# Kernel optimization log

Measured on AMD Instinct MI355X. Metric: run time of the kernel, lower is better.

## Reference

```python
import jax, jax.numpy as jnp
import numpy as np

NUM_HEADS = 8
CHUNK = 2
TAU = 2.0

# --- LIF neuron with ATan surrogate gradient (spikingjelly MultiStepLIFNode, hard reset to 0, detach_reset) ---
@jax.custom_vjp
def spike(x):
    return (x >= 0.0).astype(x.dtype)

def _spike_fwd(x):
    return spike(x), x

def _spike_bwd(x, g):
    alpha = 2.0
    sg = (alpha / 2.0) / (1.0 + (jnp.pi / 2.0 * alpha * x) ** 2)
    return (g * sg,)

spike.defvjp(_spike_fwd, _spike_bwd)

def lif(x_seq, v_th=1.0):
    # x_seq: [T, ...]; v' = v + (x - v)/tau ; spike if v' >= v_th ; hard reset v=0 (reset path detached)
    def step(v, x):
        v = v + (x - v) / TAU
        s = spike(v - v_th)
        v = v * (1.0 - jax.lax.stop_gradient(s))
        return v, s
    _, s = jax.lax.scan(step, jnp.zeros_like(x_seq[0]), x_seq)
    return s

def conv1x1_bn(x, W, scale, bias, conv_bias=None):
    # 1x1 conv over channel dim + eval-mode BN (per-channel affine)
    y = jnp.einsum('tbchw,dc->tbdhw', x, W)
    if conv_bias is not None:
        y = y + conv_bias[None, None, :, None, None]
    return y * scale[None, None, :, None, None] + bias[None, None, :, None, None]


def setup_inputs() -> dict:
    key = jax.random.key(0)
    ks = jax.random.split(key, 16)
    T, B, C, H, W = 4, 32, 512, 16, 16
    s = 1.0 / np.sqrt(C)
    return {
        'x': jax.random.normal(ks[0], (T, B, C, H, W), jnp.float32),
        'Wq': jax.random.normal(ks[1], (C, C), jnp.float32) * s,
        'q_scale': jax.random.uniform(ks[2], (C,), jnp.float32, 0.5, 1.5),
        'q_bias': jax.random.normal(ks[3], (C,), jnp.float32) * 0.1,
        'Wk': jax.random.normal(ks[4], (C, C), jnp.float32) * s,
        'k_scale': jax.random.uniform(ks[5], (C,), jnp.float32, 0.5, 1.5),
        'k_bias': jax.random.normal(ks[6], (C,), jnp.float32) * 0.1,
        'Wv': jax.random.normal(ks[7], (C, C), jnp.float32) * s,
        'v_scale': jax.random.uniform(ks[8], (C,), jnp.float32, 0.5, 1.5),
        'v_bias': jax.random.normal(ks[9], (C,), jnp.float32) * 0.1,
        'Wp': jax.random.normal(ks[10], (C, C), jnp.float32) * s,
        'bp': jax.random.normal(ks[11], (C,), jnp.float32) * 0.1,
        'p_scale': jax.random.uniform(ks[12], (C,), jnp.float32, 0.5, 1.5),
        'p_bias': jax.random.normal(ks[13], (C,), jnp.float32) * 0.1,
    }


def reference(x, Wq, q_scale, q_bias, Wk, k_scale, k_bias, Wv, v_scale, v_bias, Wp, bp, p_scale, p_bias):
    T, B, C, H, W = x.shape
    N = H * W
    hd = C // NUM_HEADS
    identity = x

    xs = lif(x)  # shortcut_lif

    def qkv_branch(W_, sc, bi):
        y = lif(conv1x1_bn(xs, W_, sc, bi))           # [T,B,C,H,W] spikes
        # flatten(3).transpose(-1,-2).reshape(...heads...).permute == split C, swap N/hd
        return jnp.swapaxes(y.reshape(T, B, NUM_HEADS, hd, N), -1, -2)  # [T,B,h,N,hd]

    q = qkv_branch(Wq, q_scale, q_bias)
    k = qkv_branch(Wk, k_scale, k_bias)
    v = qkv_branch(Wv, v_scale, v_bias)

    # STAtten: temporal chunking, linear attention q @ (k^T v)
    scaling = 1.0 / H
    nc = T // CHUNK

    def to_chunks(y):  # [T,B,h,N,hd] -> [nc,B,h,CHUNK*N,hd]
        return (y.reshape(nc, CHUNK, B, NUM_HEADS, N, hd)
                 .transpose(0, 2, 3, 1, 4, 5)
                 .reshape(nc, B, NUM_HEADS, CHUNK * N, hd))

    qc, kc, vc = to_chunks(q), to_chunks(k), to_chunks(v)
    attn = jnp.einsum('nbhsd,nbhse->nbhde', kc, vc) * scaling   # [nc,B,h,hd,hd]
    out = jnp.einsum('nbhsd,nbhde->nbhse', qc, attn)            # [nc,B,h,CHUNK*N,hd]
    out = (out.reshape(nc, B, NUM_HEADS, CHUNK, N, hd)
              .transpose(0, 3, 1, 2, 4, 5)
              .reshape(T, B, NUM_HEADS, N, hd))

    x2 = jnp.swapaxes(out, -1, -2).reshape(T, B, C, N)          # [T,B,C,N]
    x2 = lif(x2, v_th=0.5).reshape(T, B, C, H, W)               # attn_lif

    x3 = conv1x1_bn(x2, Wp, p_scale, p_bias, conv_bias=bp)      # proj conv+BN
    return x3 + identity, v
```

## Files before the change

kernel.cpp:

```cpp
#include <hip/hip_runtime.h>

typedef unsigned short ushort_t;
typedef unsigned char u8;
typedef short bf16x8 __attribute__((ext_vector_type(8)));
typedef float f32x4 __attribute__((ext_vector_type(4)));

#define T_DIM 4
#define B_DIM 32
#define C_DIM 512
#define N_DIM 256

__device__ __forceinline__ float bf2f(ushort_t u) {
  union { unsigned int i; float f; } x;
  x.i = ((unsigned int)u) << 16;
  return x.f;
}
__device__ __forceinline__ ushort_t f2bf(float f) {
  unsigned int u = __float_as_uint(f);
  u = (u + 0x7FFFu + ((u >> 16) & 1u)) >> 16;
  return (ushort_t)u;
}

__global__ __launch_bounds__(256) void k0_split(
    const float* __restrict__ Wq, const float* __restrict__ Wk,
    const float* __restrict__ Wv, const float* __restrict__ Wp,
    ushort_t* __restrict__ Sqkv, ushort_t* __restrict__ Sp)
{
  int gid = blockIdx.x * 256 + threadIdx.x;
  int w = gid >> 15;
  int off = (gid & 32767) * 8;
  const float* src = (w == 0) ? Wq : ((w == 1) ? Wk : ((w == 2) ? Wv : Wp));
  ushort_t* dst = (w < 3) ? (Sqkv + (size_t)w * 3 * 262144) : Sp;
  float wv[8];
  *(float4*)&wv[0] = *(const float4*)(src + off);
  *(float4*)&wv[4] = *(const float4*)(src + off + 4);
  ushort_t hi[8], mi[8], lo[8];
#pragma unroll
  for (int i = 0; i < 8; i++) {
    float f = wv[i];
    ushort_t h = f2bf(f);  float r  = f - bf2f(h);
    ushort_t m = f2bf(r);  float r2 = r - bf2f(m);
    ushort_t l = f2bf(r2);
    hi[i] = h; mi[i] = m; lo[i] = l;
  }
  *(uint4*)(dst + off)              = *(uint4*)&hi[0];
  *(uint4*)(dst + 262144 + off)     = *(uint4*)&mi[0];
  *(uint4*)(dst + 2 * 262144 + off) = *(uint4*)&lo[0];
}

__global__ __launch_bounds__(256) void k1_shortcut_lif(
    const float* __restrict__ x, u8* __restrict__ xsT8)
{
  const int n0 = blockIdx.x * 64;
  const int c0 = blockIdx.y * 64;
  const int b  = blockIdx.z;
  __shared__ u8 sm[64][80];
  const int tid = threadIdx.x;
  const int r  = tid >> 2;
  const int j0 = (tid & 3) * 16;
  float v[16];
#pragma unroll
  for (int i = 0; i < 16; i++) v[i] = 0.f;
  for (int t = 0; t < T_DIM; t++) {
    const float* xp = x + ((((size_t)t * B_DIM + b) * C_DIM) + c0 + r) * N_DIM + n0 + j0;
    float xv[16];
    *(float4*)&xv[0]  = *(const float4*)xp;
    *(float4*)&xv[4]  = *(const float4*)(xp + 4);
    *(float4*)&xv[8]  = *(const float4*)(xp + 8);
    *(float4*)&xv[12] = *(const float4*)(xp + 12);
    __syncthreads();
#pragma unroll
    for (int i = 0; i < 16; i++) {
      float nv = v[i] + (xv[i] - v[i]) * 0.5f;
      bool s = (nv >= 1.0f);
      v[i] = s ? 0.f : nv;
      sm[j0 + i][r] = s ? (u8)1 : (u8)0;
    }
    __syncthreads();
    union { uint4 u; u8 b[16]; } ov;
#pragma unroll
    for (int i = 0; i < 16; i++) ov.b[i] = sm[r][j0 + i];
    u8* op = xsT8 + ((((size_t)t * B_DIM + b) * N_DIM) + n0 + r) * C_DIM + c0 + j0;
    *(uint4*)op = ov.u;
  }
}

__global__ __launch_bounds__(512, 4) void k2_qkv(
    const u8* __restrict__ xsT8, const ushort_t* __restrict__ Sqkv,
    const float* __restrict__ qsc, const float* __restrict__ qbi,
    const float* __restrict__ ksc, const float* __restrict__ kbi,
    const float* __restrict__ vsc, const float* __restrict__ vbi,
    u8* __restrict__ qs8, u8* __restrict__ ks8, float* __restrict__ vout)
{
  const int nt = blockIdx.x;
  const int mt = blockIdx.y;
  const int b  = blockIdx.z;
  const int branch = mt >> 3;
  const int mloc = (mt & 7) * 64;
  const ushort_t* Ws = Sqkv + (size_t)branch * 3 * 262144;
  const float* scp = (branch == 0) ? qsc : ((branch == 1) ? ksc : vsc);
  const float* bip = (branch == 0) ? qbi : ((branch == 1) ? kbi : vbi);

  __shared__ ushort_t As3[2][3][64][32];
  __shared__ ushort_t Bs[2][128][32];

  const int tid  = threadIdx.x;
  const int lane = tid & 63;
  const int wave = tid >> 6;
  const int wrow = (wave >> 1) * 16;
  const int wcol = (wave & 1) * 64;
  const int frow = lane & 15;
  const int fsl  = lane >> 4;

  const u8* Bb0 = xsT8 + ((size_t)b * N_DIM + nt * 128) * C_DIM;

  const int ach0 = tid;
  const int ap0 = ach0 >> 8, ar0 = (ach0 & 255) >> 2, asl0 = ach0 & 3;
  const int ach1 = tid + 512;
  const int ap1 = ach1 >> 8, ar1 = (ach1 & 255) >> 2, asl1 = ach1 & 3;
  const int brow = tid >> 1, bsl0 = (tid & 1) * 2;
  uint4 pa0, pa1, pb;

#define K2_LOAD(s_) { int t_ = (s_) >> 4; int kb_ = ((s_) & 15) * 32;                     \
    pa0 = *(const uint4*)(Ws + (size_t)ap0 * 262144 + (size_t)(mloc + ar0) * 512 + kb_ + asl0 * 8); \
    if (tid < 256) {                                                                       \
      pa1 = *(const uint4*)(Ws + (size_t)ap1 * 262144 + (size_t)(mloc + ar1) * 512 + kb_ + asl1 * 8); \
      pb  = *(const uint4*)(Bb0 + (size_t)t_ * B_DIM * N_DIM * C_DIM + (size_t)brow * 512 + kb_ + bsl0 * 8); \
    } }

#define K2_WRITE(buf_) {                                                                   \
    *(uint4*)&As3[buf_][ap0][ar0][(asl0 ^ ((ar0 >> 1) & 3)) * 8] = pa0;                    \
    if (tid < 256) {                                                                       \
      *(uint4*)&As3[buf_][ap1][ar1][(asl1 ^ ((ar1 >> 1) & 3)) * 8] = pa1;                  \
      union { uint4 u; u8 bb[16]; } rw_; rw_.u = pb;                                       \
      ushort_t tmp_[16];                                                                   \
      _Pragma("unroll") for (int z_ = 0; z_ < 16; z_++) tmp_[z_] = rw_.bb[z_] ? (ushort_t)0x3F80u : (ushort_t)0u; \
      int sw_ = (brow >> 1) & 3;                                                           \
      *(uint4*)&Bs[buf_][brow][((bsl0) ^ sw_) * 8]     = *(uint4*)&tmp_[0];                \
      *(uint4*)&Bs[buf_][brow][((bsl0 + 1) ^ sw_) * 8] = *(uint4*)&tmp_[8];                \
    } }

  f32x4 acc[4];
  float vst[16];
#pragma unroll
  for (int i = 0; i < 16; i++) vst[i] = 0.f;
#pragma unroll
  for (int i = 0; i < 4; i++) acc[i] = (f32x4){0.f, 0.f, 0.f, 0.f};

  const int crow0 = (lane >> 4) * 4;
  const int cn    = lane & 15;
  float sc4[4], bi4[4];
#pragma unroll
  for (int r = 0; r < 4; r++) {
    int c = mloc + wrow + crow0 + r;
    sc4[r] = scp[c]; bi4[r] = bip[c];
  }

  K2_LOAD(0); K2_WRITE(0); __syncthreads();

  for (int s = 0; s < 64; s++) {
    const int cur = s & 1;
    if (s < 63) K2_LOAD(s + 1);
    bf16x8 bfr[4];
#pragma unroll
    for (int j = 0; j < 4; j++) {
      int row = wcol + j * 16 + frow;
      bfr[j] = *(const bf16x8*)&Bs[cur][row][(fsl ^ ((row >> 1) & 3)) * 8];
    }
    int arow = wrow + frow;
    int asw  = (fsl ^ ((arow >> 1) & 3)) * 8;
#pragma unroll
    for (int p = 0; p < 3; p++) {
      bf16x8 af = *(const bf16x8*)&As3[cur][p][arow][asw];
#pragma unroll
      for (int j = 0; j < 4; j++)
        acc[j] = __builtin_amdgcn_mfma_f32_16x16x32_bf16(af, bfr[j], acc[j], 0, 0, 0);
    }
    if (s < 63) K2_WRITE((s + 1) & 1);
    __syncthreads();

    if ((s & 15) == 15) {
      const int t = s >> 4;
      const size_t tb = (size_t)t * B_DIM + b;
      if (branch < 2) {
        u8* dst = (branch == 0) ? qs8 : ks8;
#pragma unroll
        for (int r = 0; r < 4; r++) {
          int c = mloc + wrow + crow0 + r;
#pragma unroll
          for (int j = 0; j < 4; j++) {
            int n = nt * 128 + wcol + j * 16 + cn;
            float y = acc[j][r] * sc4[r] + bi4[r];
            int vi = j * 4 + r;
            float v = vst[vi];
            v = v + (y - v) * 0.5f;
            bool sp = (v >= 1.0f);
            vst[vi] = sp ? 0.f : v;
            dst[(tb * C_DIM + c) * N_DIM + n] = sp ? (u8)1 : (u8)0;
          }
        }
      } else {
        const int hv = mloc >> 6;
        const int d0 = wrow + crow0;
#pragma unroll
        for (int j = 0; j < 4; j++) {
          int n = nt * 128 + wcol + j * 16 + cn;
          float4 o;
          float ov[4];
#pragma unroll
          for (int r = 0; r < 4; r++) {
            float y = acc[j][r] * sc4[r] + bi4[r];
            int vi = j * 4 + r;
            float v = vst[vi];
            v = v + (y - v) * 0.5f;
            bool sp = (v >= 1.0f);
            vst[vi] = sp ? 0.f : v;
            ov[r] = sp ? 1.0f : 0.0f;
          }
          o.x = ov[0]; o.y = ov[1]; o.z = ov[2]; o.w = ov[3];
          *(float4*)(vout + ((tb * 8 + hv) * N_DIM + n) * 64 + d0) = o;
        }
      }
#pragma unroll
      for (int i = 0; i < 4; i++) acc[i] = (f32x4){0.f, 0.f, 0.f, 0.f};
    }
  }
#undef K2_LOAD
#undef K2_WRITE
}

__global__ __launch_bounds__(256) void k3_attn(
    const u8* __restrict__ ks8, const float* __restrict__ vsp,
    float* __restrict__ attn)
{
  const int h  = blockIdx.x;
  const int b  = blockIdx.y;
  const int ch = blockIdx.z;
  __shared__ u8 KtT[64][80];
  __shared__ u8 Vt[64][80];
  const int tid = threadIdx.x;
  const int d0 = (tid >> 4) * 4;
  const int e0 = (tid & 15) * 4;
  float a[16];
#pragma unroll
  for (int i = 0; i < 16; i++) a[i] = 0.f;

  for (int tt = 0; tt < 2; tt++) {
    int t = ch * 2 + tt;
    for (int n0 = 0; n0 < 256; n0 += 64) {
      __syncthreads();
      {
        int d  = tid >> 2;
        int s0 = (tid & 3) * 16;
        union { uint4 u; u8 bvec[16]; } kb;
        kb.u = *(const uint4*)(ks8 + ((((size_t)t * B_DIM + b) * C_DIM) + h * 64 + d) * N_DIM + n0 + s0);
#pragma unroll
        for (int i = 0; i < 16; i++) KtT[s0 + i][d] = kb.bvec[i];
      }
      {
        const float* vb = vsp + ((((size_t)t * B_DIM + b) * 8 + h) * N_DIM + n0) * 64;
#pragma unroll
        for (int u = 0; u < 4; u++) {
          int chunk = tid + u * 256;
          int row = chunk >> 4;
          int eo  = (chunk & 15) * 4;
          float4 v4 = *(const float4*)(vb + (size_t)row * 64 + eo);
          Vt[row][eo + 0] = (u8)(v4.x != 0.f);
          Vt[row][eo + 1] = (u8)(v4.y != 0.f);
          Vt[row][eo + 2] = (u8)(v4.z != 0.f);
          Vt[row][eo + 3] = (u8)(v4.w != 0.f);
        }
      }
      __syncthreads();
      for (int s = 0; s < 64; s++) {
        uchar4 kb = *(const uchar4*)&KtT[s][d0];
        float kv[4] = { (float)kb.x, (float)kb.y, (float)kb.z, (float)kb.w };
        uchar4 vr = *(const uchar4*)&Vt[s][e0];
        float vv[4] = { (float)vr.x, (float)vr.y, (float)vr.z, (float)vr.w };
#pragma unroll
        for (int i = 0; i < 4; i++)
#pragma unroll
          for (int j = 0; j < 4; j++) a[i * 4 + j] += kv[i] * vv[j];
      }
    }
  }
  float* ap = attn + ((((size_t)ch * B_DIM + b) * 8 + h) * 64 + d0) * 64 + e0;
#pragma unroll
  for (int i = 0; i < 4; i++)
#pragma unroll
    for (int j = 0; j < 4; j++)
      ap[i * 64 + j] = a[i * 4 + j] * 0.0625f;
}

__global__ __launch_bounds__(256) void k4_out_lif(
    const u8* __restrict__ qs8, const float* __restrict__ attn,
    u8* __restrict__ x2sT8)
{
  const int h  = blockIdx.x;
  const int b  = blockIdx.y;
  const int nc = blockIdx.z;
  __shared__ float At[64][68];
  __shared__ u8 Qt[64][80];
  const int tid = threadIdx.x;
  const int e0 = (tid >> 4) * 4;
  const int n0 = (tid & 15) * 4;
  float vst[16];
#pragma unroll
  for (int i = 0; i < 16; i++) vst[i] = 0.f;

  for (int t = 0; t < T_DIM; t++) {
    if ((t & 1) == 0) {
      __syncthreads();
      const float* ap = attn + ((((size_t)(t >> 1) * B_DIM + b) * 8) + h) * 4096;
      int dr = tid >> 2;
      int co = (tid & 3) * 16;
#pragma unroll
      for (int u = 0; u < 4; u++)
        *(float4*)&At[dr][co + u * 4] = *(const float4*)(ap + dr * 64 + co + u * 4);
    }
    __syncthreads();
    {
      int d  = tid >> 2;
      int so = (tid & 3) * 16;
      *(uint4*)&Qt[d][so] =
        *(const uint4*)(qs8 + ((((size_t)t * B_DIM + b) * C_DIM) + h * 64 + d) * N_DIM + nc * 64 + so);
    }
    __syncthreads();
    float acc[16];
#pragma unroll
    for (int i = 0; i < 16; i++) acc[i] = 0.f;
    for (int d = 0; d < 64; d++) {
      float4 av = *(const float4*)&At[d][e0];
      float avv[4] = { av.x, av.y, av.z, av.w };
      uchar4 qr = *(const uchar4*)&Qt[d][n0];
      float qv[4] = { (float)qr.x, (float)qr.y, (float)qr.z, (float)qr.w };
#pragma unroll
      for (int i = 0; i < 4; i++)
#pragma unroll
        for (int j = 0; j < 4; j++) acc[i * 4 + j] += avv[i] * qv[j];
    }
#pragma unroll
    for (int j = 0; j < 4; j++) {
      u8 sv[4];
#pragma unroll
      for (int i = 0; i < 4; i++) {
        int vi = i * 4 + j;
        float y = acc[i * 4 + j];
        float nv = vst[vi] + (y - vst[vi]) * 0.5f;
        bool s = (nv >= 0.5f);
        vst[vi] = s ? 0.f : nv;
        sv[i] = s ? (u8)1 : (u8)0;
      }
      int n = nc * 64 + n0 + j;
      u8* op = x2sT8 + ((((size_t)t * B_DIM + b) * N_DIM) + n) * C_DIM + h * 64 + e0;
      *(uchar4*)op = make_uchar4(sv[0], sv[1], sv[2], sv[3]);
    }
  }
}

__global__ __launch_bounds__(512, 4) void k5_proj(
    const u8* __restrict__ x2sT8, const ushort_t* __restrict__ Sp,
    const float* __restrict__ bp, const float* __restrict__ psc,
    const float* __restrict__ pbi,
    const float* __restrict__ x, float* __restrict__ out0)
{
  const int nt = blockIdx.x;
  const int mt = blockIdx.y;
  const int tb = blockIdx.z;
  const int mloc = mt * 64;

  __shared__ ushort_t As3[2][3][64][32];
  __shared__ ushort_t Bs[2][128][32];

  const int tid  = threadIdx.x;
  const int lane = tid & 63;
  const int wave = tid >> 6;
  const int wrow = (wave >> 1) * 16;
  const int wcol = (wave & 1) * 64;
  const int frow = lane & 15;
  const int fsl  = lane >> 4;

  const u8* Bb = x2sT8 + ((size_t)tb * N_DIM + nt * 128) * C_DIM;

  const int ach0 = tid;
  const int ap0 = ach0 >> 8, ar0 = (ach0 & 255) >> 2, asl0 = ach0 & 3;
  const int ach1 = tid + 512;
  const int ap1 = ach1 >> 8, ar1 = (ach1 & 255) >> 2, asl1 = ach1 & 3;
  const int brow = tid >> 1, bsl0 = (tid & 1) * 2;
  uint4 pa0, pa1, pb;

#define K5_LOAD(s_) { int kb_ = (s_) * 32;                                                 \
    pa0 = *(const uint4*)(Sp + (size_t)ap0 * 262144 + (size_t)(mloc + ar0) * 512 + kb_ + asl0 * 8); \
    if (tid < 256) {                                                                       \
      pa1 = *(const uint4*)(Sp + (size_t)ap1 * 262144 + (size_t)(mloc + ar1) * 512 + kb_ + asl1 * 8); \
      pb  = *(const uint4*)(Bb + (size_t)brow * 512 + kb_ + bsl0 * 8);                     \
    } }

#define K5_WRITE(buf_) {                                                                   \
    *(uint4*)&As3[buf_][ap0][ar0][(asl0 ^ ((ar0 >> 1) & 3)) * 8] = pa0;                    \
    if (tid < 256) {                                                                       \
      *(uint4*)&As3[buf_][ap1][ar1][(asl1 ^ ((ar1 >> 1) & 3)) * 8] = pa1;                  \
      union { uint4 u; u8 bb[16]; } rw_; rw_.u = pb;                                       \
      ushort_t tmp_[16];                                                                   \
      _Pragma("unroll") for (int z_ = 0; z_ < 16; z_++) tmp_[z_] = rw_.bb[z_] ? (ushort_t)0x3F80u : (ushort_t)0u; \
      int sw_ = (brow >> 1) & 3;                                                           \
      *(uint4*)&Bs[buf_][brow][((bsl0) ^ sw_) * 8]     = *(uint4*)&tmp_[0];                \
      *(uint4*)&Bs[buf_][brow][((bsl0 + 1) ^ sw_) * 8] = *(uint4*)&tmp_[8];                \
    } }

  f32x4 acc[4];
#pragma unroll
  for (int i = 0; i < 4; i++) acc[i] = (f32x4){0.f, 0.f, 0.f, 0.f};

  K5_LOAD(0); K5_WRITE(0); __syncthreads();

  for (int s = 0; s < 16; s++) {
    const int cur = s & 1;
    if (s < 15) K5_LOAD(s + 1);
    bf16x8 bfr[4];
#pragma unroll
    for (int j = 0; j < 4; j++) {
      int row = wcol + j * 16 + frow;
      bfr[j] = *(const bf16x8*)&Bs[cur][row][(fsl ^ ((row >> 1) & 3)) * 8];
    }
    int arow = wrow + frow;
    int asw  = (fsl ^ ((arow >> 1) & 3)) * 8;
#pragma unroll
    for (int p = 0; p < 3; p++) {
      bf16x8 af = *(const bf16x8*)&As3[cur][p][arow][asw];
#pragma unroll
      for (int j = 0; j < 4; j++)
        acc[j] = __builtin_amdgcn_mfma_f32_16x16x32_bf16(af, bfr[j], acc[j], 0, 0, 0);
    }
    if (s < 15) K5_WRITE((s + 1) & 1);
    __syncthreads();
  }

  const int crow0 = (lane >> 4) * 4;
  const int cn    = lane & 15;
#pragma unroll
  for (int r = 0; r < 4; r++) {
    int c = mloc + wrow + crow0 + r;
    float scf = psc[c];
    float bif = pbi[c];
    float bpf = bp[c];
#pragma unroll
    for (int j = 0; j < 4; j++) {
      int n = nt * 128 + wcol + j * 16 + cn;
      size_t idx = ((size_t)tb * C_DIM + c) * N_DIM + n;
      out0[idx] = (acc[j][r] + bpf) * scf + bif + x[idx];
    }
  }
#undef K5_LOAD
#undef K5_WRITE
}

extern "C" void kernel_launch(void* const* d_in, const int* in_sizes, int n_in,
                              void* d_out, int out_size, void* d_ws, size_t ws_size,
                              hipStream_t stream) {
  const float* x   = (const float*)d_in[0];
  const float* Wq  = (const float*)d_in[1];
  const float* qsc = (const float*)d_in[2];
  const float* qbi = (const float*)d_in[3];
  const float* Wk  = (const float*)d_in[4];
  const float* ksc = (const float*)d_in[5];
  const float* kbi = (const float*)d_in[6];
  const float* Wv  = (const float*)d_in[7];
  const float* vsc = (const float*)d_in[8];
  const float* vbi = (const float*)d_in[9];
  const float* Wp  = (const float*)d_in[10];
  const float* bp  = (const float*)d_in[11];
  const float* psc = (const float*)d_in[12];
  const float* pbi = (const float*)d_in[13];

  float* out0 = (float*)d_out;
  float* out1 = out0 + 16777216;

  const size_t M16 = 16u * 1024u * 1024u;
  char* o0 = (char*)d_out;
  char* ws = (char*)d_ws;

  u8*       xsT8  = (u8*)(o0);
  u8*       qs8   = (u8*)(o0 + M16);
  u8*       ks8   = (u8*)(o0 + 2 * M16);
  ushort_t* Sqkv  = (ushort_t*)(o0 + 3 * M16);
  float*    attn  = (float*)(o0);
  u8*       x2sT8 = (u8*)(ws);
  ushort_t* Sp    = (ushort_t*)(ws + M16);

  hipLaunchKernelGGL(k0_split,        dim3(512),        dim3(256), 0, stream,
                     Wq, Wk, Wv, Wp, Sqkv, Sp);
  hipLaunchKernelGGL(k1_shortcut_lif, dim3(4, 8, 32),   dim3(256), 0, stream, x, xsT8);
  hipLaunchKernelGGL(k2_qkv,          dim3(2, 24, 32),  dim3(512), 0, stream,
                     xsT8, Sqkv, qsc, qbi, ksc, kbi, vsc, vbi, qs8, ks8, out1);
  hipLaunchKernelGGL(k3_attn,         dim3(8, 32, 2),   dim3(256), 0, stream, ks8, out1, attn);
  hipLaunchKernelGGL(k4_out_lif,      dim3(8, 32, 4),   dim3(256), 0, stream, qs8, attn, x2sT8);
  hipLaunchKernelGGL(k5_proj,         dim3(2, 8, 128),  dim3(512), 0, stream,
                     x2sT8, Sp, bp, psc, pbi, x, out0);
}
```

Before: 521.0 us.

## Use direct global-to-LDS loads and wider N tiles in QKV and proj GEMMs

Both the QKV and projection GEMM kernels now stage A and B tiles with global_load_lds (direct global-to-LDS, bypassing registers) instead of register loads followed by LDS writes. The B operand stays as u8 spikes in LDS and is expanded to bf16 at fragment-read time with perm and multiply. The N tile is doubled to 256 so each block covers the full spatial dim, which halves the grid and doubles the accumulators per wave. The XOR swizzle on LDS is dropped, which can add bank conflicts. Register pressure also rises, and the grid is smaller (768 and 1024 blocks).

```diff
diff --git a/kernel.cpp b/kernel.cpp
--- a/kernel.cpp
+++ b/kernel.cpp
@@ -19,6 +19,12 @@
   unsigned int u = __float_as_uint(f);
   u = (u + 0x7FFFu + ((u >> 16) & 1u)) >> 16;
   return (ushort_t)u;
+}
+
+__device__ __forceinline__ void gload16(const void* g, void* l) {
+  __builtin_amdgcn_global_load_lds(
+      (const __attribute__((address_space(1))) unsigned int*)g,
+      (__attribute__((address_space(3))) unsigned int*)l, 16, 0, 0);
 }
 
 __global__ __launch_bounds__(256) void k0_split(
@@ -92,60 +98,51 @@
     const float* __restrict__ vsc, const float* __restrict__ vbi,
     u8* __restrict__ qs8, u8* __restrict__ ks8, float* __restrict__ vout)
 {
-  const int nt = blockIdx.x;
-  const int mt = blockIdx.y;
-  const int b  = blockIdx.z;
+  const int mt = blockIdx.x;
+  const int b  = blockIdx.y;
   const int branch = mt >> 3;
   const int mloc = (mt & 7) * 64;
   const ushort_t* Ws = Sqkv + (size_t)branch * 3 * 262144;
   const float* scp = (branch == 0) ? qsc : ((branch == 1) ? ksc : vsc);
   const float* bip = (branch == 0) ? qbi : ((branch == 1) ? kbi : vbi);
 
-  __shared__ ushort_t As3[2][3][64][32];
-  __shared__ ushort_t Bs[2][128][32];
+  __shared__ alignas(16) ushort_t As[2][3][64][32];
+  __shared__ alignas(16) u8 Bs8[2][256][32];
 
   const int tid  = threadIdx.x;
   const int lane = tid & 63;
   const int wave = tid >> 6;
   const int wrow = (wave >> 1) * 16;
-  const int wcol = (wave & 1) * 64;
+  const int wcol = (wave & 1) * 128;
   const int frow = lane & 15;
   const int fsl  = lane >> 4;
 
-  const u8* Bb0 = xsT8 + ((size_t)b * N_DIM + nt * 128) * C_DIM;
-
-  const int ach0 = tid;
-  const int ap0 = ach0 >> 8, ar0 = (ach0 & 255) >> 2, asl0 = ach0 & 3;
-  const int ach1 = tid + 512;
-  const int ap1 = ach1 >> 8, ar1 = (ach1 & 255) >> 2, asl1 = ach1 & 3;
-  const int brow = tid >> 1, bsl0 = (tid & 1) * 2;
-  uint4 pa0, pa1, pb;
-
-#define K2_LOAD(s_) { int t_ = (s_) >> 4; int kb_ = ((s_) & 15) * 32;                     \
-    pa0 = *(const uint4*)(Ws + (size_t)ap0 * 262144 + (size_t)(mloc + ar0) * 512 + kb_ + asl0 * 8); \
-    if (tid < 256) {                                                                       \
-      pa1 = *(const uint4*)(Ws + (size_t)ap1 * 262144 + (size_t)(mloc + ar1) * 512 + kb_ + asl1 * 8); \
-      pb  = *(const uint4*)(Bb0 + (size_t)t_ * B_DIM * N_DIM * C_DIM + (size_t)brow * 512 + kb_ + bsl0 * 8); \
-    } }
-
-#define K2_WRITE(buf_) {                                                                   \
-    *(uint4*)&As3[buf_][ap0][ar0][(asl0 ^ ((ar0 >> 1) & 3)) * 8] = pa0;                    \
-    if (tid < 256) {                                                                       \
-      *(uint4*)&As3[buf_][ap1][ar1][(asl1 ^ ((ar1 >> 1) & 3)) * 8] = pa1;                  \
-      union { uint4 u; u8 bb[16]; } rw_; rw_.u = pb;                                       \
-      ushort_t tmp_[16];                                                                   \
-      _Pragma("unroll") for (int z_ = 0; z_ < 16; z_++) tmp_[z_] = rw_.bb[z_] ? (ushort_t)0x3F80u : (ushort_t)0u; \
-      int sw_ = (brow >> 1) & 3;                                                           \
-      *(uint4*)&Bs[buf_][brow][((bsl0) ^ sw_) * 8]     = *(uint4*)&tmp_[0];                \
-      *(uint4*)&Bs[buf_][brow][((bsl0 + 1) ^ sw_) * 8] = *(uint4*)&tmp_[8];                \
-    } }
-
-  f32x4 acc[4];
-  float vst[16];
-#pragma unroll
-  for (int i = 0; i < 16; i++) vst[i] = 0.f;
-#pragma unroll
-  for (int i = 0; i < 4; i++) acc[i] = (f32x4){0.f, 0.f, 0.f, 0.f};
+  const u8* Bb0 = xsT8 + (size_t)b * N_DIM * C_DIM;
+
+  const int a0p = wave >> 2, a0q = wave & 3;
+  const int arl = lane >> 2;
+  const int acl = (lane & 3) * 8;
+  const int brl = lane >> 1;
+  const int bcl = (lane & 1) * 16;
+  const int cbx = (wave < 4) ? (4 + wave) : (wave - 4);
+
+#define K2_STAGE(s_) {                                                                     \
+    const int t_ = (s_) >> 4; const int kb_ = ((s_) & 15) * 32; const int bf_ = (s_) & 1;  \
+    gload16(Ws + (size_t)a0p * 262144 + (size_t)(mloc + a0q * 16 + arl) * 512 + kb_ + acl, \
+            &As[bf_][a0p][a0q * 16][0]);                                                   \
+    if (wave < 4)                                                                          \
+      gload16(Ws + 2 * 262144 + (size_t)(mloc + wave * 16 + arl) * 512 + kb_ + acl,        \
+              &As[bf_][2][wave * 16][0]);                                                  \
+    gload16(Bb0 + (size_t)t_ * (B_DIM * N_DIM * C_DIM) + (size_t)(cbx * 32 + brl) * 512 + kb_ + bcl, \
+            &Bs8[bf_][cbx * 32][0]);                                                       \
+  }
+
+  f32x4 acc[8];
+  float vst[32];
+#pragma unroll
+  for (int i = 0; i < 32; i++) vst[i] = 0.f;
+#pragma unroll
+  for (int j = 0; j < 8; j++) acc[j] = (f32x4){0.f, 0.f, 0.f, 0.f};
 
   const int crow0 = (lane >> 4) * 4;
   const int cn    = lane & 15;
@@ -156,28 +153,31 @@
     sc4[r] = scp[c]; bi4[r] = bip[c];
   }
 
-  K2_LOAD(0); K2_WRITE(0); __syncthreads();
+  K2_STAGE(0);
+  __syncthreads();
 
   for (int s = 0; s < 64; s++) {
     const int cur = s & 1;
-    if (s < 63) K2_LOAD(s + 1);
-    bf16x8 bfr[4];
-#pragma unroll
-    for (int j = 0; j < 4; j++) {
-      int row = wcol + j * 16 + frow;
-      bfr[j] = *(const bf16x8*)&Bs[cur][row][(fsl ^ ((row >> 1) & 3)) * 8];
-    }
-    int arow = wrow + frow;
-    int asw  = (fsl ^ ((arow >> 1) & 3)) * 8;
-#pragma unroll
-    for (int p = 0; p < 3; p++) {
-      bf16x8 af = *(const bf16x8*)&As3[cur][p][arow][asw];
-#pragma unroll
-      for (int j = 0; j < 4; j++)
-        acc[j] = __builtin_amdgcn_mfma_f32_16x16x32_bf16(af, bfr[j], acc[j], 0, 0, 0);
-    }
-    if (s < 63) K2_WRITE((s + 1) & 1);
-    __syncthreads();
+    if (s < 63) K2_STAGE(s + 1);
+
+    bf16x8 af[3];
+    const int ar = wrow + frow;
+#pragma unroll
+    for (int p = 0; p < 3; p++) af[p] = *(const bf16x8*)&As[cur][p][ar][fsl * 8];
+
+#pragma unroll
+    for (int j = 0; j < 8; j++) {
+      const int row = wcol + j * 16 + frow;
+      uint2 raw = *(const uint2*)&Bs8[cur][row][fsl * 8];
+      union { bf16x8 v; unsigned int u[4]; } bu;
+      bu.u[0] = __builtin_amdgcn_perm(0u, raw.x, 0x05010400u) * 0x3F80u;
+      bu.u[1] = __builtin_amdgcn_perm(0u, raw.x, 0x07030602u) * 0x3F80u;
+      bu.u[2] = __builtin_amdgcn_perm(0u, raw.y, 0x05010400u) * 0x3F80u;
+      bu.u[3] = __builtin_amdgcn_perm(0u, raw.y, 0x07030602u) * 0x3F80u;
+#pragma unroll
+      for (int p = 0; p < 3; p++)
+        acc[j] = __builtin_amdgcn_mfma_f32_16x16x32_bf16(af[p], bu.v, acc[j], 0, 0, 0);
+    }
 
     if ((s & 15) == 15) {
       const int t = s >> 4;
@@ -186,12 +186,12 @@
         u8* dst = (branch == 0) ? qs8 : ks8;
 #pragma unroll
         for (int r = 0; r < 4; r++) {
-          int c = mloc + wrow + crow0 + r;
-#pragma unroll
-          for (int j = 0; j < 4; j++) {
-            int n = nt * 128 + wcol + j * 16 + cn;
+          const int c = mloc + wrow + crow0 + r;
+#pragma unroll
+          for (int j = 0; j < 8; j++) {
+            const int n = wcol + j * 16 + cn;
             float y = acc[j][r] * sc4[r] + bi4[r];
-            int vi = j * 4 + r;
+            const int vi = j * 4 + r;
             float v = vst[vi];
             v = v + (y - v) * 0.5f;
             bool sp = (v >= 1.0f);
@@ -203,30 +203,29 @@
         const int hv = mloc >> 6;
         const int d0 = wrow + crow0;
 #pragma unroll
-        for (int j = 0; j < 4; j++) {
-          int n = nt * 128 + wcol + j * 16 + cn;
-          float4 o;
+        for (int j = 0; j < 8; j++) {
+          const int n = wcol + j * 16 + cn;
           float ov[4];
 #pragma unroll
           for (int r = 0; r < 4; r++) {
             float y = acc[j][r] * sc4[r] + bi4[r];
-            int vi = j * 4 + r;
+            const int vi = j * 4 + r;
             float v = vst[vi];
             v = v + (y - v) * 0.5f;
             bool sp = (v >= 1.0f);
             vst[vi] = sp ? 0.f : v;
             ov[r] = sp ? 1.0f : 0.0f;
           }
-          o.x = ov[0]; o.y = ov[1]; o.z = ov[2]; o.w = ov[3];
-          *(float4*)(vout + ((tb * 8 + hv) * N_DIM + n) * 64 + d0) = o;
+          *(float4*)(vout + ((tb * 8 + hv) * N_DIM + n) * 64 + d0) =
+              make_float4(ov[0], ov[1], ov[2], ov[3]);
         }
       }
 #pragma unroll
-      for (int i = 0; i < 4; i++) acc[i] = (f32x4){0.f, 0.f, 0.f, 0.f};
-    }
-  }
-#undef K2_LOAD
-#undef K2_WRITE
+      for (int j = 0; j < 8; j++) acc[j] = (f32x4){0.f, 0.f, 0.f, 0.f};
+    }
+    __syncthreads();
+  }
+#undef K2_STAGE
 }
 
 __global__ __launch_bounds__(256) void k3_attn(
@@ -364,75 +363,69 @@
     const float* __restrict__ pbi,
     const float* __restrict__ x, float* __restrict__ out0)
 {
-  const int nt = blockIdx.x;
-  const int mt = blockIdx.y;
-  const int tb = blockIdx.z;
+  const int mt = blockIdx.x;
+  const int tb = blockIdx.y;
   const int mloc = mt * 64;
 
-  __shared__ ushort_t As3[2][3][64][32];
-  __shared__ ushort_t Bs[2][128][32];
+  __shared__ alignas(16) ushort_t As[2][3][64][32];
+  __shared__ alignas(16) u8 Bs8[2][256][32];
 
   const int tid  = threadIdx.x;
   const int lane = tid & 63;
   const int wave = tid >> 6;
   const int wrow = (wave >> 1) * 16;
-  const int wcol = (wave & 1) * 64;
+  const int wcol = (wave & 1) * 128;
   const int frow = lane & 15;
   const int fsl  = lane >> 4;
 
-  const u8* Bb = x2sT8 + ((size_t)tb * N_DIM + nt * 128) * C_DIM;
-
-  const int ach0 = tid;
-  const int ap0 = ach0 >> 8, ar0 = (ach0 & 255) >> 2, asl0 = ach0 & 3;
-  const int ach1 = tid + 512;
-  const int ap1 = ach1 >> 8, ar1 = (ach1 & 255) >> 2, asl1 = ach1 & 3;
-  const int brow = tid >> 1, bsl0 = (tid & 1) * 2;
-  uint4 pa0, pa1, pb;
-
-#define K5_LOAD(s_) { int kb_ = (s_) * 32;                                                 \
-    pa0 = *(const uint4*)(Sp + (size_t)ap0 * 262144 + (size_t)(mloc + ar0) * 512 + kb_ + asl0 * 8); \
-    if (tid < 256) {                                                                       \
-      pa1 = *(const uint4*)(Sp + (size_t)ap1 * 262144 + (size_t)(mloc + ar1) * 512 + kb_ + asl1 * 8); \
-      pb  = *(const uint4*)(Bb + (size_t)brow * 512 + kb_ + bsl0 * 8);                     \
-    } }
-
-#define K5_WRITE(buf_) {                                                                   \
-    *(uint4*)&As3[buf_][ap0][ar0][(asl0 ^ ((ar0 >> 1) & 3)) * 8] = pa0;                    \
-    if (tid < 256) {                                                                       \
-      *(uint4*)&As3[buf_][ap1][ar1][(asl1 ^ ((ar1 >> 1) & 3)) * 8] = pa1;                  \
-      union { uint4 u; u8 bb[16]; } rw_; rw_.u = pb;                                       \
-      ushort_t tmp_[16];                                                                   \
-      _Pragma("unroll") for (int z_ = 0; z_ < 16; z_++) tmp_[z_] = rw_.bb[z_] ? (ushort_t)0x3F80u : (ushort_t)0u; \
-      int sw_ = (brow >> 1) & 3;                                                           \
-      *(uint4*)&Bs[buf_][brow][((bsl0) ^ sw_) * 8]     = *(uint4*)&tmp_[0];                \
-      *(uint4*)&Bs[buf_][brow][((bsl0 + 1) ^ sw_) * 8] = *(uint4*)&tmp_[8];                \
-    } }
-
-  f32x4 acc[4];
-#pragma unroll
-  for (int i = 0; i < 4; i++) acc[i] = (f32x4){0.f, 0.f, 0.f, 0.f};
-
-  K5_LOAD(0); K5_WRITE(0); __syncthreads();
+  const u8* Bb = x2sT8 + (size_t)tb * N_DIM * C_DIM;
+
+  const int a0p = wave >> 2, a0q = wave & 3;
+  const int arl = lane >> 2;
+  const int acl = (lane & 3) * 8;
+  const int brl = lane >> 1;
+  const int bcl = (lane & 1) * 16;
+  const int cbx = (wave < 4) ? (4 + wave) : (wave - 4);
+
+#define K5_STAGE(s_) {                                                                     \
+    const int kb_ = (s_) * 32; const int bf_ = (s_) & 1;                                   \
+    gload16(Sp + (size_t)a0p * 262144 + (size_t)(mloc + a0q * 16 + arl) * 512 + kb_ + acl, \
+            &As[bf_][a0p][a0q * 16][0]);                                                   \
+    if (wave < 4)                                                                          \
+      gload16(Sp + 2 * 262144 + (size_t)(mloc + wave * 16 + arl) * 512 + kb_ + acl,        \
+              &As[bf_][2][wave * 16][0]);                                                  \
+    gload16(Bb + (size_t)(cbx * 32 + brl) * 512 + kb_ + bcl, &Bs8[bf_][cbx * 32][0]);      \
+  }
+
+  f32x4 acc[8];
+#pragma unroll
+  for (int j = 0; j < 8; j++) acc[j] = (f32x4){0.f, 0.f, 0.f, 0.f};
+
+  K5_STAGE(0);
+  __syncthreads();
 
   for (int s = 0; s < 16; s++) {
     const int cur = s & 1;
-    if (s < 15) K5_LOAD(s + 1);
-    bf16x8 bfr[4];
-#pragma unroll
-    for (int j = 0; j < 4; j++) {
-      int row = wcol + j * 16 + frow;
-      bfr[j] = *(const bf16x8*)&Bs[cur][row][(fsl ^ ((row >> 1) & 3)) * 8];
-    }
-    int arow = wrow + frow;
-    int asw  = (fsl ^ ((arow >> 1) & 3)) * 8;
-#pragma unroll
-    for (int p = 0; p < 3; p++) {
-      bf16x8 af = *(const bf16x8*)&As3[cur][p][arow][asw];
-#pragma unroll
-      for (int j = 0; j < 4; j++)
-        acc[j] = __builtin_amdgcn_mfma_f32_16x16x32_bf16(af, bfr[j], acc[j], 0, 0, 0);
-    }
-    if (s < 15) K5_WRITE((s + 1) & 1);
+    if (s < 15) K5_STAGE(s + 1);
+
+    bf16x8 af[3];
+    const int ar = wrow + frow;
+#pragma unroll
+    for (int p = 0; p < 3; p++) af[p] = *(const bf16x8*)&As[cur][p][ar][fsl * 8];
+
+#pragma unroll
+    for (int j = 0; j < 8; j++) {
+      const int row = wcol + j * 16 + frow;
+      uint2 raw = *(const uint2*)&Bs8[cur][row][fsl * 8];
+      union { bf16x8 v; unsigned int u[4]; } bu;
+      bu.u[0] = __builtin_amdgcn_perm(0u, raw.x, 0x05010400u) * 0x3F80u;
+      bu.u[1] = __builtin_amdgcn_perm(0u, raw.x, 0x07030602u) * 0x3F80u;
+      bu.u[2] = __builtin_amdgcn_perm(0u, raw.y, 0x05010400u) * 0x3F80u;
+      bu.u[3] = __builtin_amdgcn_perm(0u, raw.y, 0x07030602u) * 0x3F80u;
+#pragma unroll
+      for (int p = 0; p < 3; p++)
+        acc[j] = __builtin_amdgcn_mfma_f32_16x16x32_bf16(af[p], bu.v, acc[j], 0, 0, 0);
+    }
     __syncthreads();
   }
 
@@ -440,19 +433,18 @@
   const int cn    = lane & 15;
 #pragma unroll
   for (int r = 0; r < 4; r++) {
-    int c = mloc + wrow + crow0 + r;
-    float scf = psc[c];
-    float bif = pbi[c];
-    float bpf = bp[c];
-#pragma unroll
-    for (int j = 0; j < 4; j++) {
-      int n = nt * 128 + wcol + j * 16 + cn;
-      size_t idx = ((size_t)tb * C_DIM + c) * N_DIM + n;
+    const int c = mloc + wrow + crow0 + r;
+    const float scf = psc[c];
+    const float bif = pbi[c];
+    const float bpf = bp[c];
+#pragma unroll
+    for (int j = 0; j < 8; j++) {
+      const int n = wcol + j * 16 + cn;
+      const size_t idx = ((size_t)tb * C_DIM + c) * N_DIM + n;
       out0[idx] = (acc[j][r] + bpf) * scf + bif + x[idx];
     }
   }
-#undef K5_LOAD
-#undef K5_WRITE
+#undef K5_STAGE
 }
 
 extern "C" void kernel_launch(void* const* d_in, const int* in_sizes, int n_in,
@@ -491,10 +483,10 @@
   hipLaunchKernelGGL(k0_split,        dim3(512),        dim3(256), 0, stream,
                      Wq, Wk, Wv, Wp, Sqkv, Sp);
   hipLaunchKernelGGL(k1_shortcut_lif, dim3(4, 8, 32),   dim3(256), 0, stream, x, xsT8);
-  hipLaunchKernelGGL(k2_qkv,          dim3(2, 24, 32),  dim3(512), 0, stream,
+  hipLaunchKernelGGL(k2_qkv,          dim3(24, 32),     dim3(512), 0, stream,
                      xsT8, Sqkv, qsc, qbi, ksc, kbi, vsc, vbi, qs8, ks8, out1);
   hipLaunchKernelGGL(k3_attn,         dim3(8, 32, 2),   dim3(256), 0, stream, ks8, out1, attn);
   hipLaunchKernelGGL(k4_out_lif,      dim3(8, 32, 4),   dim3(256), 0, stream, qs8, attn, x2sT8);
-  hipLaunchKernelGGL(k5_proj,         dim3(2, 8, 128),  dim3(512), 0, stream,
+  hipLaunchKernelGGL(k5_proj,         dim3(8, 128),     dim3(512), 0, stream,
                      x2sT8, Sp, bp, psc, pbi, x, out0);
 }
```

After: 541.8 us. 4.0% more time.
